# Kernel optimization log

Measured on AMD Instinct MI355X. Metric: run time of the kernel, lower is better.

## Reference

```python
import jax, jax.numpy as jnp
import numpy as np

B, NH, T, N = 8, 12, 1024, 256
THETA = 2.0 ** 16
TWO_PI = 2.0 * np.pi


def make_freqs(n, theta):
    # RoPE frequencies in cycles (phases_cos_sin later does %1 * 2*pi)
    half = theta ** (-np.arange(0, n, 2, dtype=np.float64) / n) / TWO_PI
    return jnp.asarray(np.repeat(half, 2), dtype=jnp.float32).reshape(1, 1, 1, n)


def setup_inputs() -> dict:
    key = jax.random.key(0)
    kq, kv = jax.random.split(key)
    Q = jax.random.normal(kq, (B, NH, T, N), dtype=jnp.float32)
    V = jax.random.normal(kv, (B, NH, T, N), dtype=jnp.float32)
    return {"Q": Q, "V": V, "freqs": make_freqs(N, THETA)}


def rope(phases, v):
    ang = (phases % 1.0) * (2.0 * jnp.pi)
    cos, sin = jnp.cos(ang), jnp.sin(ang)
    # pair rotation: (even, odd) -> (-odd, even)
    v_rot = jnp.stack((-v[..., 1::2], v[..., ::2]), axis=-1).reshape(v.shape)
    return v * cos + v_rot * sin


def reference(Q, V, freqs):
    t = Q.shape[2]
    # phases: [1,1,T,1] * [1,1,1,N] -> [1,1,T,N]
    phases = jnp.arange(t, dtype=freqs.dtype).reshape(1, 1, -1, 1) * freqs
    QR = rope(phases, Q)  # KR = QR (K is Q)
    scores = jnp.einsum('bhtn,bhsn->bhts', QR, QR)
    scale = jnp.asarray(Q.shape[-1], Q.dtype) ** 0.5
    attn = jax.nn.softmax(scores / scale, axis=-1)
    return jnp.einsum('bhts,bhsn->bhtn', attn, V)
```

## Files before the change

### kernel.cpp

```cpp
#include <hip/hip_runtime.h>
#include <hip/hip_bf16.h>
#include <stdint.h>

#define B_ 8
#define NH_ 12
#define NBH (B_*NH_)
#define T_ 1024
#define D_ 256

typedef __attribute__((ext_vector_type(8))) short bf16x8;
typedef __attribute__((ext_vector_type(16))) float f32x16;
typedef unsigned short ushort_t;

#define Z16 ((f32x16){0,0,0,0,0,0,0,0,0,0,0,0,0,0,0,0})

#define KSCALE 0.30028060218f

__device__ __forceinline__ short f2bf(float x) {
  __hip_bfloat16 h = __float2bfloat16(x);
  return *reinterpret_cast<short*>(&h);
}
__device__ __forceinline__ float bf2f(short x) {
  unsigned int u = ((unsigned int)(unsigned short)x) << 16;
  return __uint_as_float(u);
}
__device__ __forceinline__ void gload16(const ushort_t* g, ushort_t* l) {
  __builtin_amdgcn_global_load_lds(
      (const __attribute__((address_space(1))) uint32_t*)g,
      (__attribute__((address_space(3))) uint32_t*)l, 16, 0, 0);
}


__global__ void tab_kernel(const float* __restrict__ freqs, float2* __restrict__ tab) {
  int idx = blockIdx.x * blockDim.x + threadIdx.x;
  if (idx >= T_ * (D_/2)) return;
  int t = idx >> 7;
  int i = idx & 127;
  float ph = (float)t * freqs[2*i];
  ph -= floorf(ph);
  float ang = ph * 6.283185307179586f;
  tab[idx] = make_float2(cosf(ang), sinf(ang));
}

__global__ __launch_bounds__(256) void kr_kernel(const float* __restrict__ Q,
                                                 const float2* __restrict__ tab,
                                                 ushort_t* __restrict__ KR) {
  int row = blockIdx.x * 8 + (threadIdx.x >> 5);
  int d8  = threadIdx.x & 31;
  int t = row & (T_ - 1);
  const float* src = Q + (size_t)row * D_ + d8 * 8;
  float4 x0 = *(const float4*)src;
  float4 x1 = *(const float4*)(src + 4);
  const float2* tr = tab + t * (D_/2) + d8 * 4;
  float2 c0 = tr[0], c1 = tr[1], c2 = tr[2], c3 = tr[3];
  bf16x8 f;
  f[0] = f2bf((x0.x * c0.x - x0.y * c0.y) * KSCALE);
  f[1] = f2bf((x0.y * c0.x + x0.x * c0.y) * KSCALE);
  f[2] = f2bf((x0.z * c1.x - x0.w * c1.y) * KSCALE);
  f[3] = f2bf((x0.w * c1.x + x0.z * c1.y) * KSCALE);
  f[4] = f2bf((x1.x * c2.x - x1.y * c2.y) * KSCALE);
  f[5] = f2bf((x1.y * c2.x + x1.x * c2.y) * KSCALE);
  f[6] = f2bf((x1.z * c3.x - x1.w * c3.y) * KSCALE);
  f[7] = f2bf((x1.w * c3.x + x1.z * c3.y) * KSCALE);
  *(bf16x8*)(KR + (size_t)row * D_ + d8 * 8) = f;
}

__global__ __launch_bounds__(256) void vt_kernel(const float* __restrict__ V,
                                                 ushort_t* __restrict__ VT) {
  int blk = blockIdx.x;
  int d64 = blk & 3, t64 = (blk >> 2) & 15, bh = blk >> 6;
  __shared__ ushort_t st[64][66];
  {
    int t = threadIdx.x >> 2, j = threadIdx.x & 3;
    const float* src = V + ((size_t)bh * T_ + t64 * 64 + t) * D_ + d64 * 64 + j * 16;
#pragma unroll
    for (int q2 = 0; q2 < 4; ++q2) {
      float4 x = *(const float4*)(src + q2 * 4);
      st[t][j*16 + q2*4 + 0] = (ushort_t)f2bf(x.x);
      st[t][j*16 + q2*4 + 1] = (ushort_t)f2bf(x.y);
      st[t][j*16 + q2*4 + 2] = (ushort_t)f2bf(x.z);
      st[t][j*16 + q2*4 + 3] = (ushort_t)f2bf(x.w);
    }
  }
  __syncthreads();
  {
    int d = threadIdx.x >> 2, tq = threadIdx.x & 3;
    bf16x8 a_, b_;
#pragma unroll
    for (int i = 0; i < 8; ++i) {
      a_[i] = (short)st[tq*16 + i][d];
      b_[i] = (short)st[tq*16 + 8 + i][d];
    }
    ushort_t* dst = VT + ((size_t)bh * D_ + d64*64 + d) * T_ + t64*64 + tq*16;
    *(bf16x8*)dst = a_;
    *(bf16x8*)(dst + 8) = b_;
  }
}

__global__ __launch_bounds__(256, 4)
void gemm1_kernel(const ushort_t* __restrict__ KRg, ushort_t* __restrict__ P) {
  int bid = blockIdx.x;
  int nblk = gridDim.x;
  int swz = (bid & 7) * (nblk >> 3) + (bid >> 3);
  int b = swz % 36;
  int h = swz / 36;
  int ti = (int)((sqrtf(8.0f * b + 1.0f) - 1.0f) * 0.5f);
  int si = b - ti * (ti + 1) / 2;

  const ushort_t* __restrict__ Kh = KRg + (size_t)h * (T_ * D_);
  ushort_t* __restrict__ Ph = P + (size_t)h * (T_ * T_);

  const int tid = threadIdx.x, lane = tid & 63, wv = tid >> 6;
  const int lo = lane & 31, hi = lane >> 5;

  __shared__ __align__(16) ushort_t SH[2 * 128 * 64];
  ushort_t* At = SH;
  ushort_t* Bt = SH + 128 * 64;

  f32x16 acc[4];
#pragma unroll
  for (int j = 0; j < 4; ++j) acc[j] = Z16;

  const ushort_t* Abase = Kh + (size_t)ti * 128 * D_;
  const ushort_t* Bbase = Kh + (size_t)si * 128 * D_;

  for (int ks = 0; ks < 4; ++ks) {
    int k0 = ks * 64;
    __syncthreads();
#pragma unroll
    for (int i = 0; i < 4; ++i) {
      int d = tid + i * 256;
      int r = d >> 3, c = d & 7;
      int srcoff = r * D_ + k0 + ((c ^ (r & 7)) * 8);
      gload16(Abase + srcoff, &At[d * 8]);
      gload16(Bbase + srcoff, &Bt[d * 8]);
    }
    __syncthreads();
    __builtin_amdgcn_s_setprio(1);
#pragma unroll
    for (int kk = 0; kk < 4; ++kk) {
      int ra = 32 * wv + lo;
      bf16x8 af = *(const bf16x8*)&At[ra * 64 + (((2*kk + hi) ^ (ra & 7)) * 8)];
#pragma unroll
      for (int j = 0; j < 4; ++j) {
        int rb = 32 * j + lo;
        bf16x8 bf_ = *(const bf16x8*)&Bt[rb * 64 + (((2*kk + hi) ^ (rb & 7)) * 8)];
        acc[j] = __builtin_amdgcn_mfma_f32_32x32x16_bf16(af, bf_, acc[j], 0, 0, 0);
      }
    }
    __builtin_amdgcn_s_setprio(0);
  }

  ushort_t pe[4][16];
#pragma unroll
  for (int j = 0; j < 4; ++j)
#pragma unroll
    for (int r = 0; r < 16; ++r)
      pe[j][r] = (ushort_t)f2bf(exp2f(acc[j][r]));

#pragma unroll
  for (int j = 0; j < 4; ++j) {
#pragma unroll
    for (int r = 0; r < 16; ++r) {
      int t = ti * 128 + 32 * wv + ((r & 3) + 8 * (r >> 2) + 4 * hi);
      int s = si * 128 + 32 * j + lo;
      Ph[(size_t)t * T_ + s] = pe[j][r];
    }
  }

  if (ti != si) {
    __syncthreads();
    ushort_t* Lt = SH;
#pragma unroll
    for (int j = 0; j < 4; ++j) {
#pragma unroll
      for (int r = 0; r < 16; ++r) {
        int trow = 32 * wv + ((r & 3) + 8 * (r >> 2) + 4 * hi);
        int scol = 32 * j + lo;
        int cc = (trow >> 3) ^ (scol & 7);
        Lt[scol * 128 + (cc << 3) + (trow & 7)] = pe[j][r];
      }
    }
    __syncthreads();
#pragma unroll
    for (int it = 0; it < 8; ++it) {
      int sr = it * 16 + (tid >> 4);
      int c  = tid & 15;
      bf16x8 vv = *(const bf16x8*)&Lt[sr * 128 + ((c ^ (sr & 7)) << 3)];
      *(bf16x8*)&Ph[(size_t)(si * 128 + sr) * T_ + ti * 128 + c * 8] = vv;
    }
  }
}

__global__ __launch_bounds__(256, 4)
void gemm2_kernel(const ushort_t* __restrict__ P, const ushort_t* __restrict__ VTg,
                  float* __restrict__ Og) {
  int bid = blockIdx.x;
  int nblk = gridDim.x;
  int swz = (bid & 7) * (nblk >> 3) + (bid >> 3);
  int di = swz & 1;
  int ti = (swz >> 1) & 7;
  int h  = swz >> 4;

  const ushort_t* __restrict__ Ph = P + (size_t)h * (T_ * T_);
  const ushort_t* __restrict__ Vh = VTg + (size_t)h * (D_ * T_);
  float* __restrict__ Oh = Og + (size_t)h * (T_ * D_);

  const int tid = threadIdx.x, lane = tid & 63, wv = tid >> 6;
  const int lo = lane & 31, hi = lane >> 5;

  __shared__ __align__(16) ushort_t At[128 * 64];
  __shared__ __align__(16) ushort_t Bt[128 * 64];
  __shared__ float lB[4][32];

  f32x16 acc[4];
#pragma unroll
  for (int j = 0; j < 4; ++j) acc[j] = Z16;
  float lsum = 0.0f;

  const ushort_t* Abase = Ph + (size_t)ti * 128 * T_;
  const ushort_t* Bbase = Vh + (size_t)di * 128 * T_;

  for (int ks = 0; ks < 16; ++ks) {
    int k0 = ks * 64;
    __syncthreads();
#pragma unroll
    for (int i = 0; i < 4; ++i) {
      int d = tid + i * 256;
      int r = d >> 3, c = d & 7;
      int srcoff = r * T_ + k0 + ((c ^ (r & 7)) * 8);
      gload16(Abase + srcoff, &At[d * 8]);
      gload16(Bbase + srcoff, &Bt[d * 8]);
    }
    __syncthreads();
    __builtin_amdgcn_s_setprio(1);
#pragma unroll
    for (int kk = 0; kk < 4; ++kk) {
      int ra = 32 * wv + lo;
      bf16x8 pf = *(const bf16x8*)&At[ra * 64 + (((2*kk + hi) ^ (ra & 7)) * 8)];
      float s01 = bf2f(pf[0]) + bf2f(pf[1]);
      float s23 = bf2f(pf[2]) + bf2f(pf[3]);
      float s45 = bf2f(pf[4]) + bf2f(pf[5]);
      float s67 = bf2f(pf[6]) + bf2f(pf[7]);
      lsum += (s01 + s23) + (s45 + s67);
#pragma unroll
      for (int j = 0; j < 4; ++j) {
        int rb = 32 * j + lo;
        bf16x8 vf = *(const bf16x8*)&Bt[rb * 64 + (((2*kk + hi) ^ (rb & 7)) * 8)];
        acc[j] = __builtin_amdgcn_mfma_f32_32x32x16_bf16(pf, vf, acc[j], 0, 0, 0);
      }
    }
    __builtin_amdgcn_s_setprio(0);
  }

  lsum += __shfl_xor(lsum, 32);
  if (hi == 0) lB[wv][lo] = lsum;
  asm volatile("s_waitcnt lgkmcnt(0)" ::: "memory");

#pragma unroll
  for (int r = 0; r < 16; ++r) {
    int crow = (r & 3) + 8 * (r >> 2) + 4 * hi;
    float inv = 1.0f / lB[wv][crow];
    int t = ti * 128 + 32 * wv + crow;
#pragma unroll
    for (int j = 0; j < 4; ++j) {
      Oh[(size_t)t * D_ + di * 128 + 32 * j + lo] = acc[j][r] * inv;
    }
  }
}

extern "C" void kernel_launch(void* const* d_in, const int* in_sizes, int n_in,
                              void* d_out, int out_size, void* d_ws, size_t ws_size,
                              hipStream_t stream) {
  const float* Q     = (const float*)d_in[0];
  const float* V     = (const float*)d_in[1];
  const float* freqs = (const float*)d_in[2];
  float* Out = (float*)d_out;

  float2* tab  = (float2*)d_ws;
  ushort_t* KR = (ushort_t*)((char*)d_ws + (1 << 20));
  ushort_t* VT = (ushort_t*)((char*)d_ws + (1 << 20) + (size_t)NBH * T_ * D_ * 2);
  ushort_t* P  = (ushort_t*)((char*)d_ws + (1 << 20) + (size_t)2 * NBH * T_ * D_ * 2);

  tab_kernel<<<(T_ * (D_/2) + 255) / 256, 256, 0, stream>>>(freqs, tab);
  kr_kernel<<<NBH * T_ / 8, 256, 0, stream>>>(Q, tab, KR);
  vt_kernel<<<NBH * 16 * 4, 256, 0, stream>>>(V, VT);

  size_t base = (1 << 20) + (size_t)2 * NBH * T_ * D_ * 2;
  size_t need1 = base + (size_t)NBH * T_ * T_ * 2;
  int ng = (ws_size >= need1) ? 1 : 2;
  int hg = NBH / ng;

  for (int g = 0; g < ng; ++g) {
    const ushort_t* KRg = KR + (size_t)g * hg * T_ * D_;
    const ushort_t* VTg = VT + (size_t)g * hg * D_ * T_;
    float* Og = Out + (size_t)g * hg * T_ * D_;
    gemm1_kernel<<<hg * 36, 256, 0, stream>>>(KRg, P);
    gemm2_kernel<<<hg * 16, 256, 0, stream>>>(P, VTg, Og);
  }
}
```

Baseline: 235.8 us.

## Double-buffer B tiles in LDS and load A fragments directly to registers

Both GEMM kernels now keep two LDS buffers for the B operand and prefetch the next k-slice while MFMAs run on the current one, with one barrier per step instead of two. The A operand (K rows for gemm1, P rows for gemm2) is read straight from global memory into register fragments, also one step ahead, so its LDS staging goes away. This is meant to hide global-load latency and cut LDS traffic and synchronization. In exchange it uses more registers for the prefetched fragments, and the direct A reads may be less coalesced.

Result: slower. 304.7 us (+29.2%).

```diff
diff --git a/kernel.cpp b/kernel.cpp
--- a/kernel.cpp
+++ b/kernel.cpp
@@ -97,6 +97,35 @@
   }
 }
 
+#define G1_ITER(KS, CUR, AF, NF)                                               \
+  {                                                                            \
+    const int ks_ = (KS);                                                      \
+    if (ks_ + 1 < 4) {                                                         \
+      _Pragma("unroll")                                                        \
+      for (int i = 0; i < 4; ++i) {                                            \
+        int d = tid + i * 256;                                                 \
+        int r = d >> 3, c = d & 7;                                             \
+        gload16(Bbase + r * D_ + (ks_ + 1) * 64 + ((c ^ (r & 7)) * 8),         \
+                &Bst[(CUR) ^ 1][d * 8]);                                       \
+      }                                                                        \
+      _Pragma("unroll")                                                        \
+      for (int kk = 0; kk < 4; ++kk)                                           \
+        NF[kk] = *(const bf16x8*)(arow + (ks_ + 1) * 64 + kk * 16);            \
+    }                                                                          \
+    __builtin_amdgcn_s_setprio(1);                                             \
+    _Pragma("unroll")                                                          \
+    for (int kk = 0; kk < 4; ++kk) {                                           \
+      _Pragma("unroll")                                                        \
+      for (int j = 0; j < 4; ++j) {                                            \
+        int rb = 32 * j + lo;                                                  \
+        bf16x8 bf_ = *(const bf16x8*)&Bst[CUR][rb * 64 + (((2*kk + hi) ^ (rb & 7)) * 8)]; \
+        acc[j] = __builtin_amdgcn_mfma_f32_32x32x16_bf16(AF[kk], bf_, acc[j], 0, 0, 0); \
+      }                                                                        \
+    }                                                                          \
+    __builtin_amdgcn_s_setprio(0);                                             \
+    __syncthreads();                                                           \
+  }
+
 __global__ __launch_bounds__(256, 4)
 void gemm1_kernel(const ushort_t* __restrict__ KRg, ushort_t* __restrict__ P) {
   int bid = blockIdx.x;
@@ -113,43 +142,30 @@
   const int tid = threadIdx.x, lane = tid & 63, wv = tid >> 6;
   const int lo = lane & 31, hi = lane >> 5;
 
-  __shared__ __align__(16) ushort_t SH[2 * 128 * 64];
-  ushort_t* At = SH;
-  ushort_t* Bt = SH + 128 * 64;
+  __shared__ __align__(16) ushort_t Bst[2][128 * 64];
 
   f32x16 acc[4];
 #pragma unroll
   for (int j = 0; j < 4; ++j) acc[j] = Z16;
 
-  const ushort_t* Abase = Kh + (size_t)ti * 128 * D_;
   const ushort_t* Bbase = Kh + (size_t)si * 128 * D_;
-
-  for (int ks = 0; ks < 4; ++ks) {
-    int k0 = ks * 64;
-    __syncthreads();
-#pragma unroll
-    for (int i = 0; i < 4; ++i) {
-      int d = tid + i * 256;
-      int r = d >> 3, c = d & 7;
-      int srcoff = r * D_ + k0 + ((c ^ (r & 7)) * 8);
-      gload16(Abase + srcoff, &At[d * 8]);
-      gload16(Bbase + srcoff, &Bt[d * 8]);
-    }
-    __syncthreads();
-    __builtin_amdgcn_s_setprio(1);
-#pragma unroll
-    for (int kk = 0; kk < 4; ++kk) {
-      int ra = 32 * wv + lo;
-      bf16x8 af = *(const bf16x8*)&At[ra * 64 + (((2*kk + hi) ^ (ra & 7)) * 8)];
-#pragma unroll
-      for (int j = 0; j < 4; ++j) {
-        int rb = 32 * j + lo;
-        bf16x8 bf_ = *(const bf16x8*)&Bt[rb * 64 + (((2*kk + hi) ^ (rb & 7)) * 8)];
-        acc[j] = __builtin_amdgcn_mfma_f32_32x32x16_bf16(af, bf_, acc[j], 0, 0, 0);
-      }
-    }
-    __builtin_amdgcn_s_setprio(0);
-  }
+  const ushort_t* arow  = Kh + (size_t)(ti * 128 + 32 * wv + lo) * D_ + hi * 8;
+
+  bf16x8 afa[4], afb[4];
+#pragma unroll
+  for (int i = 0; i < 4; ++i) {
+    int d = tid + i * 256;
+    int r = d >> 3, c = d & 7;
+    gload16(Bbase + r * D_ + ((c ^ (r & 7)) * 8), &Bst[0][d * 8]);
+  }
+#pragma unroll
+  for (int kk = 0; kk < 4; ++kk) afa[kk] = *(const bf16x8*)(arow + kk * 16);
+  __syncthreads();
+
+  G1_ITER(0, 0, afa, afb);
+  G1_ITER(1, 1, afb, afa);
+  G1_ITER(2, 0, afa, afb);
+  G1_ITER(3, 1, afb, afa);
 
   ushort_t pe[4][16];
 #pragma unroll
@@ -170,7 +186,7 @@
 
   if (ti != si) {
     __syncthreads();
-    ushort_t* Lt = SH;
+    ushort_t* Lt = &Bst[0][0];
 #pragma unroll
     for (int j = 0; j < 4; ++j) {
 #pragma unroll
@@ -191,6 +207,40 @@
     }
   }
 }
+
+#define G2_ITER(KS, CUR, PF, NF)                                               \
+  {                                                                            \
+    const int ks_ = (KS);                                                      \
+    if (ks_ + 1 < 16) {                                                        \
+      _Pragma("unroll")                                                        \
+      for (int i = 0; i < 4; ++i) {                                            \
+        int d = tid + i * 256;                                                 \
+        int r = d >> 3, c = d & 7;                                             \
+        gload16(Bbase + r * T_ + (ks_ + 1) * 64 + ((c ^ (r & 7)) * 8),         \
+                &Bst[(CUR) ^ 1][d * 8]);                                       \
+      }                                                                        \
+      _Pragma("unroll")                                                        \
+      for (int kk = 0; kk < 4; ++kk)                                           \
+        NF[kk] = *(const bf16x8*)(prow + (ks_ + 1) * 64 + kk * 16);            \
+    }                                                                          \
+    __builtin_amdgcn_s_setprio(1);                                             \
+    _Pragma("unroll")                                                          \
+    for (int kk = 0; kk < 4; ++kk) {                                           \
+      float s01 = bf2f(PF[kk][0]) + bf2f(PF[kk][1]);                           \
+      float s23 = bf2f(PF[kk][2]) + bf2f(PF[kk][3]);                           \
+      float s45 = bf2f(PF[kk][4]) + bf2f(PF[kk][5]);                           \
+      float s67 = bf2f(PF[kk][6]) + bf2f(PF[kk][7]);                           \
+      lsum += (s01 + s23) + (s45 + s67);                                       \
+      _Pragma("unroll")                                                        \
+      for (int j = 0; j < 4; ++j) {                                            \
+        int rb = 32 * j + lo;                                                  \
+        bf16x8 vf = *(const bf16x8*)&Bst[CUR][rb * 64 + (((2*kk + hi) ^ (rb & 7)) * 8)]; \
+        acc[j] = __builtin_amdgcn_mfma_f32_32x32x16_bf16(PF[kk], vf, acc[j], 0, 0, 0); \
+      }                                                                        \
+    }                                                                          \
+    __builtin_amdgcn_s_setprio(0);                                             \
+    __syncthreads();                                                           \
+  }
 
 __global__ __launch_bounds__(256, 4)
 void gemm2_kernel(const ushort_t* __restrict__ P, const ushort_t* __restrict__ VTg,
@@ -209,8 +259,7 @@
   const int tid = threadIdx.x, lane = tid & 63, wv = tid >> 6;
   const int lo = lane & 31, hi = lane >> 5;
 
-  __shared__ __align__(16) ushort_t At[128 * 64];
-  __shared__ __align__(16) ushort_t Bt[128 * 64];
+  __shared__ __align__(16) ushort_t Bst[2][128 * 64];
   __shared__ float lB[4][32];
 
   f32x16 acc[4];
@@ -218,39 +267,23 @@
   for (int j = 0; j < 4; ++j) acc[j] = Z16;
   float lsum = 0.0f;
 
-  const ushort_t* Abase = Ph + (size_t)ti * 128 * T_;
   const ushort_t* Bbase = Vh + (size_t)di * 128 * T_;
-
-  for (int ks = 0; ks < 16; ++ks) {
-    int k0 = ks * 64;
-    __syncthreads();
-#pragma unroll
-    for (int i = 0; i < 4; ++i) {
-      int d = tid + i * 256;
-      int r = d >> 3, c = d & 7;
-      int srcoff = r * T_ + k0 + ((c ^ (r & 7)) * 8);
-      gload16(Abase + srcoff, &At[d * 8]);
-      gload16(Bbase + srcoff, &Bt[d * 8]);
-    }
-    __syncthreads();
-    __builtin_amdgcn_s_setprio(1);
-#pragma unroll
-    for (int kk = 0; kk < 4; ++kk) {
-      int ra = 32 * wv + lo;
-      bf16x8 pf = *(const bf16x8*)&At[ra * 64 + (((2*kk + hi) ^ (ra & 7)) * 8)];
-      float s01 = bf2f(pf[0]) + bf2f(pf[1]);
-      float s23 = bf2f(pf[2]) + bf2f(pf[3]);
-      float s45 = bf2f(pf[4]) + bf2f(pf[5]);
-      float s67 = bf2f(pf[6]) + bf2f(pf[7]);
-      lsum += (s01 + s23) + (s45 + s67);
-#pragma unroll
-      for (int j = 0; j < 4; ++j) {
-        int rb = 32 * j + lo;
-        bf16x8 vf = *(const bf16x8*)&Bt[rb * 64 + (((2*kk + hi) ^ (rb & 7)) * 8)];
-        acc[j] = __builtin_amdgcn_mfma_f32_32x32x16_bf16(pf, vf, acc[j], 0, 0, 0);
-      }
-    }
-    __builtin_amdgcn_s_setprio(0);
+  const ushort_t* prow  = Ph + (size_t)(ti * 128 + 32 * wv + lo) * T_ + hi * 8;
+
+  bf16x8 pfa[4], pfb[4];
+#pragma unroll
+  for (int i = 0; i < 4; ++i) {
+    int d = tid + i * 256;
+    int r = d >> 3, c = d & 7;
+    gload16(Bbase + r * T_ + ((c ^ (r & 7)) * 8), &Bst[0][d * 8]);
+  }
+#pragma unroll
+  for (int kk = 0; kk < 4; ++kk) pfa[kk] = *(const bf16x8*)(prow + kk * 16);
+  __syncthreads();
+
+  for (int t2 = 0; t2 < 16; t2 += 2) {
+    G2_ITER(t2,     0, pfa, pfb);
+    G2_ITER(t2 + 1, 1, pfb, pfa);
   }
 
   lsum += __shfl_xor(lsum, 32);
```

## Double-buffer LDS tiles in gemm2 to overlap global loads with MFMA

Applied to the files above, without the earlier changes.

Splits the P and V^T shared-memory tiles in gemm2 into ping-pong buffers. The next k-slice is loaded while MFMAs run on the current one, leaving one barrier per k-step instead of two. This targets the load-then-compute stall of the single-buffered loop. LDS per block doubles, and launch bounds drop from 4 to 2 blocks per CU, which lowers occupancy and could cancel the latency hiding.

Measured after the change: 234.1 us (median of 2 runs). About the same (-0.7%).

```diff
diff --git a/kernel.cpp b/kernel.cpp
--- a/kernel.cpp
+++ b/kernel.cpp
@@ -192,7 +192,44 @@
   }
 }
 
-__global__ __launch_bounds__(256, 4)
+#define G2_STAGE(KS, PD, VD)                                                   \
+  {                                                                            \
+    int k0_ = (KS) * 64;                                                       \
+    _Pragma("unroll")                                                          \
+    for (int i = 0; i < 4; ++i) {                                              \
+      int dd = tid + i * 256;                                                  \
+      int r = dd >> 3, c = dd & 7;                                             \
+      int off_ = r * T_ + k0_ + ((c ^ (r & 7)) * 8);                           \
+      gload16(Abase + off_, &PD[dd * 8]);                                      \
+      gload16(Bbase + off_, &VD[dd * 8]);                                      \
+    }                                                                          \
+  }
+
+#define G2_ITER(TT, PC, VC, PN, VN)                                            \
+  {                                                                            \
+    if ((TT) + 1 < 16) G2_STAGE((TT) + 1, PN, VN);                             \
+    __builtin_amdgcn_s_setprio(1);                                             \
+    _Pragma("unroll")                                                          \
+    for (int kk = 0; kk < 4; ++kk) {                                           \
+      int ra = 32 * wv + lo;                                                   \
+      bf16x8 pf = *(const bf16x8*)&PC[ra * 64 + (((2*kk + hi) ^ (ra & 7)) * 8)]; \
+      float s01 = bf2f(pf[0]) + bf2f(pf[1]);                                   \
+      float s23 = bf2f(pf[2]) + bf2f(pf[3]);                                   \
+      float s45 = bf2f(pf[4]) + bf2f(pf[5]);                                   \
+      float s67 = bf2f(pf[6]) + bf2f(pf[7]);                                   \
+      lsum += (s01 + s23) + (s45 + s67);                                       \
+      _Pragma("unroll")                                                        \
+      for (int j = 0; j < 4; ++j) {                                            \
+        int rb = 32 * j + lo;                                                  \
+        bf16x8 vf = *(const bf16x8*)&VC[rb * 64 + (((2*kk + hi) ^ (rb & 7)) * 8)]; \
+        acc[j] = __builtin_amdgcn_mfma_f32_32x32x16_bf16(pf, vf, acc[j], 0, 0, 0); \
+      }                                                                        \
+    }                                                                          \
+    __builtin_amdgcn_s_setprio(0);                                             \
+    __syncthreads();                                                           \
+  }
+
+__global__ __launch_bounds__(256, 2)
 void gemm2_kernel(const ushort_t* __restrict__ P, const ushort_t* __restrict__ VTg,
                   float* __restrict__ Og) {
   int bid = blockIdx.x;
@@ -209,8 +246,10 @@
   const int tid = threadIdx.x, lane = tid & 63, wv = tid >> 6;
   const int lo = lane & 31, hi = lane >> 5;
 
-  __shared__ __align__(16) ushort_t At[128 * 64];
-  __shared__ __align__(16) ushort_t Bt[128 * 64];
+  __shared__ __align__(16) ushort_t Pa[128 * 64];
+  __shared__ __align__(16) ushort_t Pb[128 * 64];
+  __shared__ __align__(16) ushort_t Va[128 * 64];
+  __shared__ __align__(16) ushort_t Vb[128 * 64];
   __shared__ float lB[4][32];
 
   f32x16 acc[4];
@@ -221,36 +260,12 @@
   const ushort_t* Abase = Ph + (size_t)ti * 128 * T_;
   const ushort_t* Bbase = Vh + (size_t)di * 128 * T_;
 
-  for (int ks = 0; ks < 16; ++ks) {
-    int k0 = ks * 64;
-    __syncthreads();
-#pragma unroll
-    for (int i = 0; i < 4; ++i) {
-      int d = tid + i * 256;
-      int r = d >> 3, c = d & 7;
-      int srcoff = r * T_ + k0 + ((c ^ (r & 7)) * 8);
-      gload16(Abase + srcoff, &At[d * 8]);
-      gload16(Bbase + srcoff, &Bt[d * 8]);
-    }
-    __syncthreads();
-    __builtin_amdgcn_s_setprio(1);
-#pragma unroll
-    for (int kk = 0; kk < 4; ++kk) {
-      int ra = 32 * wv + lo;
-      bf16x8 pf = *(const bf16x8*)&At[ra * 64 + (((2*kk + hi) ^ (ra & 7)) * 8)];
-      float s01 = bf2f(pf[0]) + bf2f(pf[1]);
-      float s23 = bf2f(pf[2]) + bf2f(pf[3]);
-      float s45 = bf2f(pf[4]) + bf2f(pf[5]);
-      float s67 = bf2f(pf[6]) + bf2f(pf[7]);
-      lsum += (s01 + s23) + (s45 + s67);
-#pragma unroll
-      for (int j = 0; j < 4; ++j) {
-        int rb = 32 * j + lo;
-        bf16x8 vf = *(const bf16x8*)&Bt[rb * 64 + (((2*kk + hi) ^ (rb & 7)) * 8)];
-        acc[j] = __builtin_amdgcn_mfma_f32_32x32x16_bf16(pf, vf, acc[j], 0, 0, 0);
-      }
-    }
-    __builtin_amdgcn_s_setprio(0);
+  G2_STAGE(0, Pa, Va);
+  __syncthreads();
+
+  for (int t2 = 0; t2 < 16; t2 += 2) {
+    G2_ITER(t2,     Pa, Va, Pb, Vb);
+    G2_ITER(t2 + 1, Pb, Vb, Pa, Va);
   }
 
   lsum += __shfl_xor(lsum, 32);
```
